# Kernel tuning notes

Measured on AMD Instinct MI355X. Metric: run time of the kernel, lower is better.

## Reference

```python
import jax, jax.numpy as jnp
import numpy as np

T, N, D = 2048, 64, 1024
EPS = 1e-6  # torch gaussian_nll_loss var clamp
HALF_LOG_2PI = 0.5 * float(np.log(2.0 * np.pi))


def setup_inputs() -> dict:
    key = jax.random.key(0)
    k1, k2, k3, k4 = jax.random.split(key, 4)
    x = jax.random.normal(k1, (T, N, D), dtype=jnp.float32)
    y = jax.random.normal(k2, (T, N), dtype=jnp.float32)
    # Linear(in_size, 2, bias=False) weight, kaiming-uniform-ish scale
    W = jax.random.normal(k3, (2, D), dtype=jnp.float32) / np.sqrt(D)
    # per-sequence lengths in [1, T], sorted descending (PackedSequence convention)
    lens = jnp.sort(jax.random.randint(k4, (N,), 1, T + 1))[::-1].astype(jnp.int32)
    return {"y": y, "x": x, "W": W, "lens": lens}


def reference(y, x, W, lens):
    # b[t, n] = position t is valid for sequence n (prefix mask == packed mask)
    Tt, Nn = y.shape
    b = jnp.arange(Tt, dtype=jnp.int32)[:, None] < lens[None, :]  # (T, N) bool
    # tiny 2-output linear over all positions (dense + mask == masked_select + linear)
    out = jnp.einsum('tnd,kd->tnk', x, W)  # (T, N, 2)
    mu = out[..., 0]
    var = jnp.maximum(jax.nn.sigmoid(out[..., 1]), EPS)
    # gaussian_nll_loss(input=y, target=mu, var=var, full=True)
    nll = 0.5 * (jnp.log(var) + (y - mu) ** 2 / var) + HALF_LOG_2PI
    nll = jnp.where(b, nll, 0.0)
    # per-sequence segment sum over time (pad_packed + sum(1))
    return nll.sum(axis=0)  # (N,)
```

## Files before the change

kernel.cpp:

```cpp
#include <hip/hip_runtime.h>
#include <math.h>

#define T_DIM 2048
#define N_DIM 64
#define D_DIM 1024
#define TC    16
#define CHUNKS (T_DIM / TC)
#define EPS 1e-6f
#define HALF_LOG_2PI 0.91893853320467274178f

__global__ void zero_out_kernel(float* out) {
    out[threadIdx.x] = 0.0f;
}

__global__ __launch_bounds__(256) void gnll_kernel(
    const float* __restrict__ y,
    const float* __restrict__ x,
    const float* __restrict__ W,
    const int*   __restrict__ lens,
    float*       __restrict__ out)
{
    const int lane = threadIdx.x & 63;
    const int wave = threadIdx.x >> 6;
    const int wg   = blockIdx.x * 4 + wave;
    const int n     = wg & (N_DIM - 1);
    const int chunk = wg >> 6;
    const int len = lens[n];
    const int t0 = chunk * TC;
    if (t0 >= len) return;
    const int t1 = min(t0 + TC, len);

    const int half = lane >> 5;
    const int c    = lane & 31;

    const float4* W0 = (const float4*)W;
    const float4* W1 = (const float4*)(W + D_DIM);
    float4 w0[8], w1[8];
#pragma unroll
    for (int j = 0; j < 8; ++j) {
        w0[j] = W0[j * 32 + c];
        w1[j] = W1[j * 32 + c];
    }

    float acc = 0.0f;
    for (int t2 = t0; t2 < t1; t2 += 2) {
        const int t = t2 + half;
        const float4* xr = (const float4*)(x + ((size_t)t * N_DIM + n) * D_DIM) + c;
        float m = 0.0f, s = 0.0f;
#pragma unroll
        for (int j = 0; j < 8; ++j) {
            float4 xv = xr[j * 32];
            m += xv.x * w0[j].x + xv.y * w0[j].y + xv.z * w0[j].z + xv.w * w0[j].w;
            s += xv.x * w1[j].x + xv.y * w1[j].y + xv.z * w1[j].z + xv.w * w1[j].w;
        }
#pragma unroll
        for (int off = 16; off > 0; off >>= 1) {
            m += __shfl_xor(m, off, 64);
            s += __shfl_xor(s, off, 64);
        }
        const float yv   = y[(size_t)t * N_DIM + n];
        const float sg   = 1.0f / (1.0f + __expf(-s));
        const float var  = fmaxf(sg, EPS);
        const float diff = yv - m;
        const float nll  = 0.5f * (__logf(var) + diff * diff / var) + HALF_LOG_2PI;
        const bool valid = (t < len) && (c == 0);
        acc += valid ? nll : 0.0f;
    }
    acc += __shfl_xor(acc, 32, 64);
    if (lane == 0) atomicAdd(out + n, acc);
}

extern "C" void kernel_launch(void* const* d_in, const int* in_sizes, int n_in,
                              void* d_out, int out_size, void* d_ws, size_t ws_size,
                              hipStream_t stream) {
    const float* y    = (const float*)d_in[0];
    const float* x    = (const float*)d_in[1];
    const float* W    = (const float*)d_in[2];
    const int*   lens = (const int*)d_in[3];
    float* out = (float*)d_out;

    zero_out_kernel<<<1, N_DIM, 0, stream>>>(out);
    gnll_kernel<<<(N_DIM * CHUNKS) / 4, 256, 0, stream>>>(y, x, W, lens, out);
}
```

Baseline: 640.1 us.

## Map each wave to two adjacent sequences and fully unroll the time block

Each wave now handles two neighbouring sequences (one per half-wave) over a 16-step time block, where before it handled a single sequence over two time steps at a time. Within a time step, the two half-waves read adjacent rows of x, so a wave touches 8KB of contiguous memory. Full time blocks are fully unrolled so many loads can be in flight at once. The cost is wasted work on padded steps of the shorter sequence in each pair, plus higher register pressure from the unroll.

Measured after the change: 641.8 us. Within noise of the previous version (+0.3%).

```diff
diff --git a/kernel.cpp b/kernel.cpp
--- a/kernel.cpp
+++ b/kernel.cpp
@@ -4,8 +4,9 @@
 #define T_DIM 2048
 #define N_DIM 64
 #define D_DIM 1024
-#define TC    16
-#define CHUNKS (T_DIM / TC)
+#define TB    16
+#define TBLKS (T_DIM / TB)
+#define NPAIRS (N_DIM / 2)
 #define EPS 1e-6f
 #define HALF_LOG_2PI 0.91893853320467274178f
 
@@ -23,15 +24,17 @@
     const int lane = threadIdx.x & 63;
     const int wave = threadIdx.x >> 6;
     const int wg   = blockIdx.x * 4 + wave;
-    const int n     = wg & (N_DIM - 1);
-    const int chunk = wg >> 6;
-    const int len = lens[n];
-    const int t0 = chunk * TC;
-    if (t0 >= len) return;
-    const int t1 = min(t0 + TC, len);
-
+    const int pair = wg & (NPAIRS - 1);
+    const int tblk = wg >> 5;
     const int half = lane >> 5;
     const int c    = lane & 31;
+    const int n    = 2 * pair + half;
+
+    const int t0     = tblk * TB;
+    const int len_hi = lens[2 * pair];
+    if (t0 >= len_hi) return;
+    const int t1    = min(t0 + TB, len_hi);
+    const int len_n = lens[n];
 
     const float4* W0 = (const float4*)W;
     const float4* W1 = (const float4*)(W + D_DIM);
@@ -42,32 +45,48 @@
         w1[j] = W1[j * 32 + c];
     }
 
+    const size_t TSTR = (size_t)N_DIM * (D_DIM / 4);
+    const float4* xp = (const float4*)(x + ((size_t)t0 * N_DIM + n) * D_DIM) + c;
+
     float acc = 0.0f;
-    for (int t2 = t0; t2 < t1; t2 += 2) {
-        const int t = t2 + half;
-        const float4* xr = (const float4*)(x + ((size_t)t * N_DIM + n) * D_DIM) + c;
-        float m = 0.0f, s = 0.0f;
+
+#define BODY(T_IDX, PTR) do {                                                  \
+        float m = 0.0f, s = 0.0f;                                              \
+        _Pragma("unroll")                                                      \
+        for (int j = 0; j < 8; ++j) {                                          \
+            const float4 xv = (PTR)[j * 32];                                   \
+            m += xv.x * w0[j].x + xv.y * w0[j].y                               \
+               + xv.z * w0[j].z + xv.w * w0[j].w;                              \
+            s += xv.x * w1[j].x + xv.y * w1[j].y                               \
+               + xv.z * w1[j].z + xv.w * w1[j].w;                              \
+        }                                                                      \
+        _Pragma("unroll")                                                      \
+        for (int off = 16; off > 0; off >>= 1) {                               \
+            m += __shfl_xor(m, off, 64);                                       \
+            s += __shfl_xor(s, off, 64);                                       \
+        }                                                                      \
+        const float yv   = y[(size_t)(T_IDX) * N_DIM + n];                     \
+        const float sg   = 1.0f / (1.0f + __expf(-s));                         \
+        const float var  = fmaxf(sg, EPS);                                     \
+        const float diff = yv - m;                                             \
+        const float nll  = 0.5f * (__logf(var) + diff * diff / var)            \
+                         + HALF_LOG_2PI;                                       \
+        acc += (((T_IDX) < len_n) & (c == 0)) ? nll : 0.0f;                    \
+    } while (0)
+
+    if (t1 - t0 == TB) {
 #pragma unroll
-        for (int j = 0; j < 8; ++j) {
-            float4 xv = xr[j * 32];
-            m += xv.x * w0[j].x + xv.y * w0[j].y + xv.z * w0[j].z + xv.w * w0[j].w;
-            s += xv.x * w1[j].x + xv.y * w1[j].y + xv.z * w1[j].z + xv.w * w1[j].w;
+        for (int i = 0; i < TB; ++i) {
+            BODY(t0 + i, xp + (size_t)i * TSTR);
         }
-#pragma unroll
-        for (int off = 16; off > 0; off >>= 1) {
-            m += __shfl_xor(m, off, 64);
-            s += __shfl_xor(s, off, 64);
+    } else {
+        for (int t = t0; t < t1; ++t, xp += TSTR) {
+            BODY(t, xp);
         }
-        const float yv   = y[(size_t)t * N_DIM + n];
-        const float sg   = 1.0f / (1.0f + __expf(-s));
-        const float var  = fmaxf(sg, EPS);
-        const float diff = yv - m;
-        const float nll  = 0.5f * (__logf(var) + diff * diff / var) + HALF_LOG_2PI;
-        const bool valid = (t < len) && (c == 0);
-        acc += valid ? nll : 0.0f;
     }
-    acc += __shfl_xor(acc, 32, 64);
-    if (lane == 0) atomicAdd(out + n, acc);
+#undef BODY
+
+    if (c == 0) atomicAdd(out + n, acc);
 }
 
 extern "C" void kernel_launch(void* const* d_in, const int* in_sizes, int n_in,
@@ -80,5 +99,5 @@
     float* out = (float*)d_out;
 
     zero_out_kernel<<<1, N_DIM, 0, stream>>>(out);
-    gnll_kernel<<<(N_DIM * CHUNKS) / 4, 256, 0, stream>>>(y, x, W, lens, out);
+    gnll_kernel<<<(NPAIRS * TBLKS) / 4, 256, 0, stream>>>(y, x, W, lens, out);
 }
```
